# Optimization experiments

Hardware: AMD Instinct MI355X
Metric: run time of the kernel (lower is better)

Reference implementation:

```python
import math
import jax, jax.numpy as jnp
import numpy as np

D_MODEL = 1024
N_HEADS = 16
D_K = D_MODEL // N_HEADS
THETA = 10000.0


def setup_inputs() -> dict:
    key = jax.random.key(0)
    k1, k2, k3 = jax.random.split(key, 3)
    B, S = 2, 2048
    x = jax.random.normal(k1, (B, S, D_MODEL), dtype=jnp.float32)
    std_qkv = math.sqrt(2.0 / (D_MODEL + 3 * D_MODEL))
    std_out = math.sqrt(2.0 / (D_MODEL + D_MODEL))
    # Linear weights stored as (out_features, in_features) to match the
    # einsum '... i, o i -> ... o' contraction (trunc-normal approximated
    # by clipped normal for the reference baseline).
    w_qkv = jnp.clip(jax.random.normal(k2, (3 * D_MODEL, D_MODEL), dtype=jnp.float32) * std_qkv,
                     -3 * std_qkv, 3 * std_qkv)
    b_qkv = jnp.zeros((3 * D_MODEL,), dtype=jnp.float32)
    w_out = jnp.clip(jax.random.normal(k3, (D_MODEL, D_MODEL), dtype=jnp.float32) * std_out,
                     -3 * std_out, 3 * std_out)
    b_out = jnp.zeros((D_MODEL,), dtype=jnp.float32)
    return {"x": x, "w_qkv": w_qkv, "b_qkv": b_qkv, "w_out": w_out, "b_out": b_out}


def _rope(t, cos, sin):
    # t: (B, H, S, D_K); cos/sin: (S, D_K//2) broadcast over batch/heads.
    B, H, S, d = t.shape
    tp = t.reshape(B, H, S, d // 2, 2)
    even, odd = tp[..., 0], tp[..., 1]
    r_even = even * cos - odd * sin
    r_odd = even * sin + odd * cos
    return jnp.stack([r_even, r_odd], axis=-1).reshape(B, H, S, d)


def reference(x, w_qkv, b_qkv, w_out, b_out):
    B, S, _ = x.shape
    # QKV projection: weight is (out, in)
    qkv = jnp.einsum('bsi,oi->bso', x, w_qkv) + b_qkv  # (B, S, 3*D_MODEL)
    qkv = qkv.reshape(B, S, 3, N_HEADS, D_K).transpose(2, 0, 3, 1, 4)  # (3, B, H, S, D_K)
    q, k, v = qkv[0], qkv[1], qkv[2]

    # RoPE with default token_positions = arange(S)
    inv_freq = THETA ** (-(jnp.arange(0, D_K, 2, dtype=jnp.float32)) / D_K)  # (D_K//2,)
    ang = jnp.arange(S, dtype=jnp.float32)[:, None] * inv_freq[None, :]      # (S, D_K//2)
    cos, sin = jnp.cos(ang), jnp.sin(ang)
    q = _rope(q, cos, sin)
    k = _rope(k, cos, sin)

    # Scaled dot-product attention in fp32 with causal mask
    scale = 1.0 / math.sqrt(D_K)
    scores = jnp.einsum('bhqd,bhkd->bhqk', q.astype(jnp.float32), k.astype(jnp.float32)) * scale
    causal = jnp.tril(jnp.ones((S, S), dtype=bool))
    scores = jnp.where(causal, scores, jnp.finfo(jnp.float32).min)
    # Custom softmax: exp(x - max) / (sum + 1e-8)
    ex = jnp.exp(scores - jnp.max(scores, axis=-1, keepdims=True))
    attn = ex / (jnp.sum(ex, axis=-1, keepdims=True) + 1e-8)
    attn = attn.astype(v.dtype)

    o = jnp.einsum('bhqk,bhkd->bhqd', attn, v)           # (B, H, S, D_K)
    o = o.transpose(0, 2, 1, 3).reshape(B, S, D_MODEL)    # (B, S, D_MODEL)
    out = jnp.einsum('bsi,oi->bso', o, w_out) + b_out
    return out
```

## Files before the change

### kernel.cpp

```cpp
#include <hip/hip_runtime.h>


typedef float f32x4 __attribute__((ext_vector_type(4)));
typedef float fvec4 __attribute__((ext_vector_type(4)));
typedef __bf16 bf16x8 __attribute__((ext_vector_type(8)));
typedef unsigned int u32x4 __attribute__((ext_vector_type(4)));

#define S_SZ 2048
#define NH 16
#define DK 64

static __device__ __forceinline__ unsigned short f2bf(float f) {
  unsigned int u = __builtin_bit_cast(unsigned int, f);
  u += 0x7fffu + ((u >> 16) & 1u);
  return (unsigned short)(u >> 16);
}
static __device__ __forceinline__ float bf2f(unsigned short h) {
  unsigned int u = ((unsigned int)h) << 16;
  return __builtin_bit_cast(float, u);
}
static __device__ __forceinline__ unsigned int pk2(float a, float b) {
  return (unsigned int)f2bf(a) | ((unsigned int)f2bf(b) << 16);
}
static __device__ __forceinline__ bf16x8 ld16g(const unsigned short* p) {
  return __builtin_bit_cast(bf16x8, *(const u32x4*)p);
}
static __device__ __forceinline__ void gload_lds16(const unsigned short* g,
                                                   unsigned short* l) {
  __builtin_amdgcn_global_load_lds(
      (const __attribute__((address_space(1))) void*)g,
      (__attribute__((address_space(3))) void*)l, 16, 0, 0);
}
static __device__ __forceinline__ float ex2(float x) {
  float r;
  asm("v_exp_f32 %0, %1" : "=v"(r) : "v"(x));
  return r;
}
static __device__ __forceinline__ unsigned int cvtpk(float a, float b) {
  unsigned int r;
  asm("v_cvt_pk_bf16_f32 %0, %1, %2" : "=v"(r) : "v"(a), "v"(b));
  return r;
}

template <int CTRL>
static __device__ __forceinline__ float dppmov(float x) {
  return __builtin_bit_cast(
      float, __builtin_amdgcn_update_dpp(0, __builtin_bit_cast(int, x), CTRL,
                                         0xF, 0xF, true));
}
static __device__ __forceinline__ float rmax16(float x) {
  x = fmaxf(x, dppmov<0xB1>(x));
  x = fmaxf(x, dppmov<0x4E>(x));
  x = fmaxf(x, dppmov<0x141>(x));
  x = fmaxf(x, dppmov<0x140>(x));
  return x;
}
static __device__ __forceinline__ float rsum16(float x) {
  x += dppmov<0xB1>(x);
  x += dppmov<0x4E>(x);
  x += dppmov<0x141>(x);
  x += dppmov<0x140>(x);
  return x;
}

__global__ __launch_bounds__(256) void cvt_bf16(
    const float* __restrict__ x, const float* __restrict__ wq,
    const float* __restrict__ wo, unsigned short* __restrict__ xb,
    unsigned short* __restrict__ wqb, unsigned short* __restrict__ wob) {
  const int u = blockIdx.x * 256 + threadIdx.x;
  const float* src;
  unsigned short* dst;
  int idx;
  if (u < 524288) { src = x; dst = xb; idx = u; }
  else if (u < 917504) { src = wq; dst = wqb; idx = u - 524288; }
  else { src = wo; dst = wob; idx = u - 917504; }
  const fvec4* p = (const fvec4*)(src + (size_t)idx * 8);
  const fvec4 f0 = p[0], f1 = p[1];
  u32x4 o;
  o[0] = pk2(f0[0], f0[1]); o[1] = pk2(f0[2], f0[3]);
  o[2] = pk2(f1[0], f1[1]); o[3] = pk2(f1[2], f1[3]);
  *(u32x4*)(dst + (size_t)idx * 8) = o;
}

template <bool OBF16>
__global__ __launch_bounds__(256) void gemm_bf16(
    const unsigned short* __restrict__ A, const unsigned short* __restrict__ B,
    const float* __restrict__ bias, void* __restrict__ Cp, int N, int K) {
  __shared__ unsigned short As[2][4096];
  __shared__ unsigned short Bs[2][4096];
  const int t = threadIdx.x;
  const int lane = t & 63, w = t >> 6;
  const int lo = lane & 15, g = lane >> 4;
  const int wr = (w >> 1) * 64, wc = (w & 1) * 64;
  const int gx = gridDim.x;
  int o = blockIdx.y * gx + blockIdx.x;
  const int nwg = gx * gridDim.y;
  o = (o & 7) * (nwg >> 3) + (o >> 3);
  const int by = o / gx, bx = o - by * gx;
  const int bRow = by * 128, bCol = bx * 128;
  const unsigned short* ap = A + (size_t)(bRow + (t >> 2)) * K + (t & 3) * 8;
  const unsigned short* bp = B + (size_t)(bCol + (t >> 2)) * K + (t & 3) * 8;
  const size_t rK = (size_t)64 * K;
  const int wb = w * 512;
  f32x4 acc[4][4] = {};
  gload_lds16(ap, As[0] + wb);
  gload_lds16(ap + rK, As[0] + 2048 + wb);
  gload_lds16(bp, Bs[0] + wb);
  gload_lds16(bp + rK, Bs[0] + 2048 + wb);
  const int nk = K >> 5;
  for (int kt = 0; kt < nk; ++kt) {
    __syncthreads();
    if (kt + 1 < nk) {
      const int k0 = (kt + 1) << 5;
      const int nb = (kt + 1) & 1;
      gload_lds16(ap + k0, As[nb] + wb);
      gload_lds16(ap + rK + k0, As[nb] + 2048 + wb);
      gload_lds16(bp + k0, Bs[nb] + wb);
      gload_lds16(bp + rK + k0, Bs[nb] + 2048 + wb);
    }
    const unsigned short* Ac = As[kt & 1];
    const unsigned short* Bc = Bs[kt & 1];
    bf16x8 aF[4], bF[4];
#pragma unroll
    for (int m = 0; m < 4; ++m) aF[m] = ld16g(Ac + (wr + m * 16 + lo) * 32 + 8 * g);
#pragma unroll
    for (int n = 0; n < 4; ++n) bF[n] = ld16g(Bc + (wc + n * 16 + lo) * 32 + 8 * g);
    __builtin_amdgcn_s_setprio(1);
#pragma unroll
    for (int m = 0; m < 4; ++m)
#pragma unroll
      for (int n = 0; n < 4; ++n)
        acc[m][n] = __builtin_amdgcn_mfma_f32_16x16x32_bf16(aF[m], bF[n], acc[m][n], 0, 0, 0);
    __builtin_amdgcn_s_setprio(0);
  }
#pragma unroll
  for (int m = 0; m < 4; ++m) {
#pragma unroll
    for (int n = 0; n < 4; ++n) {
      const int col = bCol + wc + n * 16 + lo;
      const float bv = bias[col];
#pragma unroll
      for (int r = 0; r < 4; ++r) {
        const int row = bRow + wr + m * 16 + g * 4 + r;
        const float v = acc[m][n][r] + bv;
        if constexpr (OBF16)
          ((unsigned short*)Cp)[(size_t)row * N + col] = f2bf(v);
        else
          ((float*)Cp)[(size_t)row * N + col] = v;
      }
    }
  }
}

__global__ __launch_bounds__(256) void rope_scatter(
    const unsigned short* __restrict__ qkv, unsigned short* __restrict__ Qo,
    unsigned short* __restrict__ Ko, unsigned short* __restrict__ Vt) {
  const int t = blockIdx.x * 256 + threadIdx.x;
  const int i = t & 31;
  const int s = (t >> 5) & (S_SZ - 1);
  const int h = (t >> 16) & (NH - 1);
  const int b = t >> 20;
  const unsigned short* row = qkv + (size_t)(b * S_SZ + s) * 3072;
  const float inv = exp2f((float)i * (-13.287712379549449f / 32.0f));
  const float ang = (float)s * inv;
  float sn, cs;
  sincosf(ang, &sn, &cs);
  const unsigned int qp = *(const unsigned int*)(row + h * 64 + 2 * i);
  const unsigned int kp = *(const unsigned int*)(row + 1024 + h * 64 + 2 * i);
  const unsigned int vp = *(const unsigned int*)(row + 2048 + h * 64 + 2 * i);
  const float qe = bf2f((unsigned short)qp), qo = bf2f((unsigned short)(qp >> 16));
  const float ke = bf2f((unsigned short)kp), ko = bf2f((unsigned short)(kp >> 16));
  const size_t hb = (size_t)(b * NH + h);
  const size_t qkbase = (hb * S_SZ + s) * DK + 2 * i;
  const float qs = 0.18033688011112042f;
  *(unsigned int*)(Qo + qkbase) =
      pk2((qe * cs - qo * sn) * qs, (qe * sn + qo * cs) * qs);
  *(unsigned int*)(Ko + qkbase) = pk2(ke * cs - ko * sn, ke * sn + ko * cs);
  const size_t vb = (hb * DK + 2 * i) * S_SZ + s;
  Vt[vb] = (unsigned short)vp;
  Vt[vb + S_SZ] = (unsigned short)(vp >> 16);
}

static __device__ __forceinline__ void stage8(const unsigned short* __restrict__ gbase,
                                              int gstride, unsigned short* tile, int t) {
  const int r = t >> 3;
  const int s16 = (t & 7) ^ (r & 7);
  gload_lds16(gbase + (size_t)r * gstride + (s16 << 3), tile + (t >> 6) * 512);
}

static __device__ __forceinline__ void attn_step(
    const unsigned short* __restrict__ Kl, const unsigned short* __restrict__ Vl,
    unsigned short* __restrict__ Pw, const bf16x8 aQ0, const bf16x8 aQ1,
    const bool diag, const int wq, const int lo, const int g,
    float* __restrict__ m, float* __restrict__ lsum, f32x4* __restrict__ oacc) {
  f32x4 s[4];
  __builtin_amdgcn_s_setprio(1);
#pragma unroll
  for (int c = 0; c < 4; ++c) {
    const int kr = c * 16 + lo;
    const int sw = kr & 7;
    const bf16x8 b0 =
        __builtin_bit_cast(bf16x8, *(const u32x4*)&Kl[kr * 64 + ((g ^ sw) << 3)]);
    const bf16x8 b1 =
        __builtin_bit_cast(bf16x8, *(const u32x4*)&Kl[kr * 64 + (((4 + g) ^ sw) << 3)]);
    f32x4 z = {};
    z = __builtin_amdgcn_mfma_f32_16x16x32_bf16(aQ0, b0, z, 0, 0, 0);
    z = __builtin_amdgcn_mfma_f32_16x16x32_bf16(aQ1, b1, z, 0, 0, 0);
    s[c] = z;
  }
  __builtin_amdgcn_s_setprio(0);
  if (diag) {
#pragma unroll
    for (int c = 0; c < 4; ++c)
#pragma unroll
      for (int r = 0; r < 4; ++r)
        if ((c * 16 + lo) > (wq * 16 + g * 4 + r)) s[c][r] = -__builtin_inff();
  }
  float rm[4];
#pragma unroll
  for (int r = 0; r < 4; ++r) {
    const float v = fmaxf(fmaxf(s[0][r], s[1][r]), fmaxf(s[2][r], s[3][r]));
    rm[r] = rmax16(v);
  }
  const bool grow = (rm[0] > m[0] + 8.f) | (rm[1] > m[1] + 8.f) |
                    (rm[2] > m[2] + 8.f) | (rm[3] > m[3] + 8.f);
  if (__any((int)grow)) {
#pragma unroll
    for (int r = 0; r < 4; ++r) {
      const float mn = fmaxf(m[r], rm[r]);
      const float alpha = ex2(m[r] - mn);
      m[r] = mn;
      lsum[r] *= alpha;
#pragma unroll
      for (int nt = 0; nt < 4; ++nt) oacc[nt][r] *= alpha;
    }
  }
#pragma unroll
  for (int r = 0; r < 4; ++r) {
    float rs = 0.f;
#pragma unroll
    for (int c = 0; c < 4; ++c) {
      const float p = ex2(s[c][r] - m[r]);
      s[c][r] = p;
      rs += p;
    }
    lsum[r] += rsum16(rs);
    const unsigned int u01 = cvtpk(s[0][r], s[1][r]);
    const unsigned int u23 = cvtpk(s[2][r], s[3][r]);
    unsigned short* pr = Pw + (g * 4 + r) * 72 + lo;
    pr[0] = (unsigned short)u01;
    pr[16] = (unsigned short)(u01 >> 16);
    pr[32] = (unsigned short)u23;
    pr[48] = (unsigned short)(u23 >> 16);
  }
  __builtin_amdgcn_s_setprio(1);
#pragma unroll
  for (int kc = 0; kc < 2; ++kc) {
    const bf16x8 aP =
        __builtin_bit_cast(bf16x8, *(const u32x4*)&Pw[lo * 72 + kc * 32 + 8 * g]);
#pragma unroll
    for (int nt = 0; nt < 4; ++nt) {
      const int d = nt * 16 + lo;
      const bf16x8 bV = __builtin_bit_cast(
          bf16x8, *(const u32x4*)&Vl[d * 64 + (((kc * 4 + g) ^ (d & 7)) << 3)]);
      oacc[nt] = __builtin_amdgcn_mfma_f32_16x16x32_bf16(aP, bV, oacc[nt], 0, 0, 0);
    }
  }
  __builtin_amdgcn_s_setprio(0);
}

__global__ __launch_bounds__(512, 4) void flash_attn(
    const unsigned short* __restrict__ Q, const unsigned short* __restrict__ K,
    const unsigned short* __restrict__ VT, unsigned short* __restrict__ O) {
  __shared__ unsigned short Kb[2][4096];
  __shared__ unsigned short Vb[2][4096];
  __shared__ unsigned short Pl[8][1152];
  const int t = threadIdx.x;
  const int lane = t & 63, w = t >> 6;
  const int lo = lane & 15, g = lane >> 4;
  const int flat = blockIdx.y * 16 + blockIdx.x;
  const int bh = ((flat & 7) << 2) | ((flat >> 3) & 3);
  const int j = flat >> 5;
  const int qa = j, qb = 31 - j;
  const unsigned short* Qh = Q + (size_t)bh * S_SZ * DK;
  const unsigned short* Kh = K + (size_t)bh * S_SZ * DK;
  const unsigned short* Vh = VT + (size_t)bh * DK * S_SZ;

  const int wq = w & 3;
  const bool s1 = w >= 4;
  const int rowMain = (s1 ? qb : qa) * 64 + wq * 16;
  const int rowB = qb * 64 + wq * 16;
  const bf16x8 aQ0 = ld16g(Qh + (size_t)(rowMain + lo) * DK + 8 * g);
  const bf16x8 aQ1 = ld16g(Qh + (size_t)(rowMain + lo) * DK + 32 + 8 * g);
  bf16x8 aQB0 = aQ0, aQB1 = aQ1;
  if (!s1) {
    aQB0 = ld16g(Qh + (size_t)(rowB + lo) * DK + 8 * g);
    aQB1 = ld16g(Qh + (size_t)(rowB + lo) * DK + 32 + 8 * g);
  }

  float mA[4], lA[4], mB[4], lB[4];
  f32x4 oA[4] = {}, oB[4] = {};
#pragma unroll
  for (int r = 0; r < 4; ++r) {
    mA[r] = mB[r] = -__builtin_inff();
    lA[r] = lB[r] = 0.f;
  }
  unsigned short* Pw = &Pl[w][0];

  for (int i = 0; i <= 16; ++i) {
    if (i < 16) {
      stage8(Kh + (size_t)i * 64 * DK, DK, Kb[1], t);
      stage8(Vh + i * 64, S_SZ, Vb[1], t);
    }
    if (i > qa) {
      const int t0c = 15 + i - qa;
      stage8(Kh + (size_t)t0c * 64 * DK, DK, Kb[0], t);
      stage8(Vh + t0c * 64, S_SZ, Vb[0], t);
    }
    __syncthreads();
    if (s1) {
      if (i < 16) {
        attn_step(Kb[1], Vb[1], Pw, aQ0, aQ1, false, wq, lo, g, mA, lA, oA);
      } else {
        float* ml = (float*)Pw;
#pragma unroll
        for (int r = 0; r < 4; ++r) {
          ml[r * 64 + lane] = mA[r];
          ml[(4 + r) * 64 + lane] = lA[r];
        }
        float* obase = (w < 6) ? ((float*)&Kb[1][0]) + (w - 4) * 1024
                               : ((float*)&Vb[1][0]) + (w - 6) * 1024;
#pragma unroll
        for (int nt = 0; nt < 4; ++nt)
#pragma unroll
          for (int r = 0; r < 4; ++r) obase[(nt * 4 + r) * 64 + lane] = oA[nt][r];
      }
    } else {
      if (i <= qa)
        attn_step(Kb[1], Vb[1], Pw, aQ0, aQ1, i == qa, wq, lo, g, mA, lA, oA);
      else
        attn_step(Kb[0], Vb[0], Pw, aQB0, aQB1, i == 16, wq, lo, g, mB, lB, oB);
    }
    __syncthreads();
  }

  if (!s1) {
    const int b = bh >> 4, h = bh & 15;
#pragma unroll
    for (int r = 0; r < 4; ++r) {
      const float inv = 1.0f / (lA[r] + 1e-8f);
      const size_t base = ((size_t)(b * S_SZ + rowMain + g * 4 + r)) * 1024 + h * DK;
#pragma unroll
      for (int nt = 0; nt < 4; ++nt) O[base + nt * 16 + lo] = f2bf(oA[nt][r] * inv);
    }
    const float* ml = (const float*)&Pl[w + 4][0];
    const float* obase = (w < 2) ? ((const float*)&Kb[1][0]) + w * 1024
                                 : ((const float*)&Vb[1][0]) + (w - 2) * 1024;
#pragma unroll
    for (int r = 0; r < 4; ++r) {
      const float m1 = ml[r * 64 + lane], l1 = ml[(4 + r) * 64 + lane];
      const float mh = fmaxf(mB[r], m1);
      const float a0 = ex2(mB[r] - mh), a1 = ex2(m1 - mh);
      const float linv = 1.0f / (lB[r] * a0 + l1 * a1 + 1e-8f);
      const size_t base = ((size_t)(b * S_SZ + rowB + g * 4 + r)) * 1024 + h * DK;
#pragma unroll
      for (int nt = 0; nt < 4; ++nt)
        O[base + nt * 16 + lo] =
            f2bf((oB[nt][r] * a0 + obase[(nt * 4 + r) * 64 + lane] * a1) * linv);
    }
  }
}

extern "C" void kernel_launch(void* const* d_in, const int* in_sizes, int n_in,
                              void* d_out, int out_size, void* d_ws, size_t ws_size,
                              hipStream_t stream) {
  const float* x = (const float*)d_in[0];
  const float* w_qkv = (const float*)d_in[1];
  const float* b_qkv = (const float*)d_in[2];
  const float* w_out = (const float*)d_in[3];
  const float* b_out = (const float*)d_in[4];
  float* out = (float*)d_out;

  char* ws = (char*)d_ws;
  unsigned short* xb = (unsigned short*)(ws);
  unsigned short* wqb = (unsigned short*)(ws + 8388608);
  unsigned short* wob = (unsigned short*)(ws + 14680064);
  unsigned short* qkv = (unsigned short*)(ws + 16777216);
  unsigned short* kb = (unsigned short*)(ws + 41943040);
  unsigned short* vt = (unsigned short*)(ws + 50331648);
  unsigned short* qb = xb;
  unsigned short* ob = qkv;

  cvt_bf16<<<4096, 256, 0, stream>>>(x, w_qkv, w_out, xb, wqb, wob);
  {
    dim3 grid(3072 / 128, 4096 / 128);
    gemm_bf16<true><<<grid, 256, 0, stream>>>(xb, wqb, b_qkv, qkv, 3072, 1024);
  }
  rope_scatter<<<(2 * NH * S_SZ * 32) / 256, 256, 0, stream>>>(qkv, qb, kb, vt);
  {
    dim3 grid(16, 2 * NH);
    flash_attn<<<grid, 512, 0, stream>>>(qb, kb, vt, ob);
  }
  {
    dim3 grid(1024 / 128, 4096 / 128);
    gemm_bf16<false><<<grid, 256, 0, stream>>>(ob, wob, b_out, out, 1024, 1024);
  }
}
```

Measured before the change: 138.1 us.

## Replace QKV GEMM with 256x256-tile, 8-wave, 8-phase pipelined kernel

Adds a dedicated QKV projection GEMM that uses 256x256 output tiles with 512 threads per block. Each K-step is split into four half-tile phases, so the LDS fragment loads, async global-to-LDS staging of the next tile and MFMAs are interleaved behind explicit vmcnt waits and barriers. The larger tile is meant to raise arithmetic intensity and overlap memory traffic with compute. The cost is heavy LDS use (64KB per block) and more registers, and the grid shrinks to 192 blocks, which is fewer than the CU count, so occupancy and load balance may suffer.

```diff
diff --git a/kernel.cpp b/kernel.cpp
--- a/kernel.cpp
+++ b/kernel.cpp
@@ -61,6 +61,13 @@
   x += dppmov<0x141>(x);
   x += dppmov<0x140>(x);
   return x;
+}
+
+static __device__ __forceinline__ void stage8(const unsigned short* __restrict__ gbase,
+                                              int gstride, unsigned short* tile, int t) {
+  const int r = t >> 3;
+  const int s16 = (t & 7) ^ (r & 7);
+  gload_lds16(gbase + (size_t)r * gstride + (s16 << 3), tile + (t >> 6) * 512);
 }
 
 __global__ __launch_bounds__(256) void cvt_bf16(
@@ -80,6 +87,108 @@
   o[0] = pk2(f0[0], f0[1]); o[1] = pk2(f0[2], f0[3]);
   o[2] = pk2(f1[0], f1[1]); o[3] = pk2(f1[2], f1[3]);
   *(u32x4*)(dst + (size_t)idx * 8) = o;
+}
+
+#define G1N 3072
+#define G1K 1024
+__global__ __launch_bounds__(512, 2) void gemm_qkv_8p(
+    const unsigned short* __restrict__ A, const unsigned short* __restrict__ B,
+    const float* __restrict__ bias, unsigned short* __restrict__ C) {
+  __shared__ unsigned short As[2][2][8192];
+  __shared__ unsigned short Bs[2][2][8192];
+  const int t = threadIdx.x;
+  const int lane = t & 63;
+  const int w = t >> 6;
+  const int lo = lane & 15, g = lane >> 4;
+  const int wr2 = w >> 2, wc4 = w & 3;
+  int o = blockIdx.y * 12 + blockIdx.x;
+  o = (o & 7) * 24 + (o >> 3);
+  const int by = o / 12, bx = o - by * 12;
+  const int bRow = by * 256, bCol = bx * 256;
+
+  f32x4 acc[2][2][4][2] = {};
+  bf16x8 aF[4][2], bF[2][2];
+  const int arow = wr2 * 64 + lo;
+  const int brow = wc4 * 32 + lo;
+  const int sw = lo & 7;
+
+#define STA(buf, H, k0)                                                     \
+  {                                                                         \
+    const unsigned short* gp = A + (size_t)(bRow + (H) * 128) * G1K + (k0); \
+    stage8(gp, G1K, &As[buf][H][0], t);                                     \
+    stage8(gp + (size_t)64 * G1K, G1K, &As[buf][H][4096], t);               \
+  }
+#define STB(buf, H, k0)                                                     \
+  {                                                                         \
+    const unsigned short* gp = B + (size_t)(bCol + (H) * 128) * G1K + (k0); \
+    stage8(gp, G1K, &Bs[buf][H][0], t);                                     \
+    stage8(gp + (size_t)64 * G1K, G1K, &Bs[buf][H][4096], t);               \
+  }
+#define LDA(cur, MH)                                                        \
+  _Pragma("unroll") for (int mf = 0; mf < 4; ++mf)                          \
+      _Pragma("unroll") for (int ks = 0; ks < 2; ++ks) aF[mf][ks] =         \
+      __builtin_bit_cast(bf16x8,                                            \
+          *(const u32x4*)&As[cur][MH][(arow + mf * 16) * 64 +               \
+                                      (((ks * 4 + g) ^ sw) << 3)]);
+#define LDB(cur, NHh)                                                       \
+  _Pragma("unroll") for (int nf = 0; nf < 2; ++nf)                          \
+      _Pragma("unroll") for (int ks = 0; ks < 2; ++ks) bF[nf][ks] =         \
+      __builtin_bit_cast(bf16x8,                                            \
+          *(const u32x4*)&Bs[cur][NHh][(brow + nf * 16) * 64 +              \
+                                       (((ks * 4 + g) ^ sw) << 3)]);
+#define MM(MH, NHh)                                                         \
+  __builtin_amdgcn_s_setprio(1);                                            \
+  _Pragma("unroll") for (int mf = 0; mf < 4; ++mf)                          \
+      _Pragma("unroll") for (int nf = 0; nf < 2; ++nf)                      \
+          _Pragma("unroll") for (int ks = 0; ks < 2; ++ks) acc[MH][NHh][mf] \
+      [nf] = __builtin_amdgcn_mfma_f32_16x16x32_bf16(                       \
+          aF[mf][ks], bF[nf][ks], acc[MH][NHh][mf][nf], 0, 0, 0);           \
+  __builtin_amdgcn_s_setprio(0);
+#define VM4 asm volatile("s_waitcnt vmcnt(4)" ::: "memory")
+#define VM2 asm volatile("s_waitcnt vmcnt(2)" ::: "memory")
+#define VM0 asm volatile("s_waitcnt vmcnt(0)" ::: "memory")
+#define BARR                      \
+  __builtin_amdgcn_s_barrier();   \
+  __builtin_amdgcn_sched_barrier(0)
+
+  STA(0, 0, 0) STB(0, 0, 0) STB(0, 1, 0) STA(0, 1, 0)
+
+  for (int kt = 0; kt < 15; ++kt) {
+    const int cur = kt & 1, nxt = cur ^ 1;
+    const int k1 = (kt + 1) * 64;
+    VM4; BARR; LDA(cur, 0) LDB(cur, 0) STA(nxt, 0, k1) MM(0, 0)
+    VM4; BARR; LDB(cur, 1) STB(nxt, 0, k1) MM(0, 1)
+    VM4; BARR; LDA(cur, 1) LDB(cur, 0) STB(nxt, 1, k1) MM(1, 0)
+    BARR; LDB(cur, 1) STA(nxt, 1, k1) MM(1, 1)
+  }
+  {
+    VM4; BARR; LDA(1, 0) LDB(1, 0) MM(0, 0)
+    VM2; BARR; LDB(1, 1) MM(0, 1)
+    VM0; BARR; LDA(1, 1) LDB(1, 0) MM(1, 0)
+    BARR; LDB(1, 1) MM(1, 1)
+  }
+
+#pragma unroll
+  for (int MH = 0; MH < 2; ++MH)
+#pragma unroll
+    for (int NHh = 0; NHh < 2; ++NHh)
+#pragma unroll
+      for (int mf = 0; mf < 4; ++mf)
+#pragma unroll
+        for (int nf = 0; nf < 2; ++nf) {
+          const int col = bCol + NHh * 128 + wc4 * 32 + nf * 16 + lo;
+          const float bv = bias[col];
+#pragma unroll
+          for (int rr = 0; rr < 4; ++rr) {
+            const int row = bRow + MH * 128 + wr2 * 64 + mf * 16 + g * 4 + rr;
+            C[(size_t)row * G1N + col] = f2bf(acc[MH][NHh][mf][nf][rr] + bv);
+          }
+        }
+#undef STA
+#undef STB
+#undef LDA
+#undef LDB
+#undef MM
 }
 
 template <bool OBF16>
@@ -181,13 +290,6 @@
   Vt[vb + S_SZ] = (unsigned short)(vp >> 16);
 }
 
-static __device__ __forceinline__ void stage8(const unsigned short* __restrict__ gbase,
-                                              int gstride, unsigned short* tile, int t) {
-  const int r = t >> 3;
-  const int s16 = (t & 7) ^ (r & 7);
-  gload_lds16(gbase + (size_t)r * gstride + (s16 << 3), tile + (t >> 6) * 512);
-}
-
 static __device__ __forceinline__ void attn_step(
     const unsigned short* __restrict__ Kl, const unsigned short* __restrict__ Vl,
     unsigned short* __restrict__ Pw, const bf16x8 aQ0, const bf16x8 aQ1,
@@ -393,8 +495,8 @@
 
   cvt_bf16<<<4096, 256, 0, stream>>>(x, w_qkv, w_out, xb, wqb, wob);
   {
-    dim3 grid(3072 / 128, 4096 / 128);
-    gemm_bf16<true><<<grid, 256, 0, stream>>>(xb, wqb, b_qkv, qkv, 3072, 1024);
+    dim3 grid(3072 / 256, 4096 / 256);
+    gemm_qkv_8p<<<grid, 512, 0, stream>>>(xb, wqb, b_qkv, qkv);
   }
   rope_scatter<<<(2 * NH * S_SZ * 32) / 256, 256, 0, stream>>>(qkv, qb, kb, vt);
   {
```

After: 141.6 us. 2.5% more time.
